# Kernel optimization log

Hardware: AMD Instinct MI355X
Metric: run time of the kernel (lower is better)

## Reference

```python
import jax, jax.numpy as jnp
import numpy as np

B, SQ, SKV, D = 16, 4096, 4096, 64

def setup_inputs() -> dict:
    key = jax.random.key(0)
    kq, kk, kv, ks = jax.random.split(key, 4)
    return {
        "q": jax.random.normal(kq, (B, SQ, D), dtype=jnp.float32),
        "k": jax.random.normal(kk, (B, SKV, D), dtype=jnp.float32),
        "v": jax.random.normal(kv, (B, SKV, D), dtype=jnp.float32),
        "scale_factor": jax.random.uniform(ks, (1,), dtype=jnp.float32, minval=0.05, maxval=0.2),
    }

def reference(q, k, v, scale_factor):
    # qk = q @ k^T, then divide by inv_scale = 1/scale  ==  multiply by scale
    scores = jnp.einsum("bqd,bkd->bqk", q, k) * scale_factor[0]  # [B, SQ, SKV]
    probs = jax.nn.softmax(scores, axis=-1)
    # dropout p=0.0 -> identity (source's p=1 would zero the output; see notes)
    out = jnp.einsum("bqk,bkd->bqd", probs, v)  # [B, SQ, D]
    return out
```

## Files before the change

### kernel.cpp

```cpp
#include <hip/hip_runtime.h>
#include <hip/hip_bf16.h>

#define BATCH 16
#define SEQ   4096
#define DH    64
#define KVB   64
#define NT    (SEQ / KVB)
#define LDK   72

using frag   = __attribute__((ext_vector_type(8))) short;
using f32x16 = __attribute__((ext_vector_type(16))) float;
using u16x8  = __attribute__((ext_vector_type(8))) unsigned short;

__device__ __forceinline__ unsigned short f2bf(float x) {
    union { __hip_bfloat16 h; unsigned short u; } cv;
    cv.h = __float2bfloat16(x);
    return cv.u;
}
__device__ __forceinline__ float bf2f(unsigned short u) {
    union { unsigned int i; float f; } cv;
    cv.i = ((unsigned int)u) << 16;
    return cv.f;
}
__device__ __forceinline__ float fast_exp2(float x) {
#if __has_builtin(__builtin_amdgcn_exp2f)
    return __builtin_amdgcn_exp2f(x);
#else
    float r; asm("v_exp_f32 %0, %1" : "=v"(r) : "v"(x)); return r;
#endif
}
__device__ __forceinline__ unsigned int cvtpk_bf16(float lo, float hi) {
    unsigned int r;
    asm("v_cvt_pk_bf16_f32 %0, %1, %2" : "=v"(r) : "v"(lo), "v"(hi));
    return r;
}
__device__ __forceinline__ void glds16(const unsigned short* g, unsigned short* l) {
    __builtin_amdgcn_global_load_lds(
        (const __attribute__((address_space(1))) void*)g,
        (__attribute__((address_space(3))) void*)l, 16, 0, 0);
}
__device__ __forceinline__ f32x16 mfma32(frag a, frag b, f32x16 c) {
    return __builtin_amdgcn_mfma_f32_32x32x16_bf16(a, b, c, 0, 0, 0);
}

__global__ __launch_bounds__(256) void cvt_k_frag(const float* __restrict__ K,
                                                  unsigned short* __restrict__ Kws) {
    __shared__ unsigned short Ls[64 * LDK];
    const int b = blockIdx.x >> 6;
    const int t = blockIdx.x & 63;
    const int i = threadIdx.x;
    {
        const int kv = i >> 2, db = (i & 3) * 16;
        const float* src = K + ((size_t)b * SEQ + (size_t)t * 64 + kv) * DH + db;
        float4 a = *(const float4*)(src);
        float4 c = *(const float4*)(src + 4);
        float4 d = *(const float4*)(src + 8);
        float4 e = *(const float4*)(src + 12);
        u16x8 w0, w1;
        w0[0]=f2bf(a.x); w0[1]=f2bf(a.y); w0[2]=f2bf(a.z); w0[3]=f2bf(a.w);
        w0[4]=f2bf(c.x); w0[5]=f2bf(c.y); w0[6]=f2bf(c.z); w0[7]=f2bf(c.w);
        w1[0]=f2bf(d.x); w1[1]=f2bf(d.y); w1[2]=f2bf(d.z); w1[3]=f2bf(d.w);
        w1[4]=f2bf(e.x); w1[5]=f2bf(e.y); w1[6]=f2bf(e.z); w1[7]=f2bf(e.w);
        *(u16x8*)&Ls[kv * LDK + db]     = w0;
        *(u16x8*)&Ls[kv * LDK + db + 8] = w1;
    }
    __syncthreads();
    {
        const int flat0 = i * 2;
        const int f     = flat0 >> 6;
        const int kb    = f & 1, kstep = f >> 1;
        const int l0    = flat0 & 63, l1 = l0 + 1;
        u16x8 o0 = *(const u16x8*)&Ls[(kb*32 + (l0&31)) * LDK + kstep*16 + (l0>>5)*8];
        u16x8 o1 = *(const u16x8*)&Ls[(kb*32 + (l1&31)) * LDK + kstep*16 + (l1>>5)*8];
        unsigned short* dst = Kws + ((((size_t)b*64 + t)*8 + f)*64 + l0)*8;
        *(u16x8*)dst       = o0;
        *(u16x8*)(dst + 8) = o1;
    }
}

__global__ __launch_bounds__(256) void tr_v_frag(const float* __restrict__ V,
                                                 unsigned short* __restrict__ Vws) {
    __shared__ unsigned short Ls[64 * LDK];
    const int b = blockIdx.x >> 6;
    const int t = blockIdx.x & 63;
    const int i = threadIdx.x;
    {
        const int kv = i >> 2, db = (i & 3) * 16;
        const float* src = V + ((size_t)b * SEQ + (size_t)t * 64 + kv) * DH + db;
        float4 a = *(const float4*)(src);
        float4 c = *(const float4*)(src + 4);
        float4 d = *(const float4*)(src + 8);
        float4 e = *(const float4*)(src + 12);
        u16x8 w0, w1;
        w0[0]=f2bf(a.x); w0[1]=f2bf(a.y); w0[2]=f2bf(a.z); w0[3]=f2bf(a.w);
        w0[4]=f2bf(c.x); w0[5]=f2bf(c.y); w0[6]=f2bf(c.z); w0[7]=f2bf(c.w);
        w1[0]=f2bf(d.x); w1[1]=f2bf(d.y); w1[2]=f2bf(d.z); w1[3]=f2bf(d.w);
        w1[4]=f2bf(e.x); w1[5]=f2bf(e.y); w1[6]=f2bf(e.z); w1[7]=f2bf(e.w);
        *(u16x8*)&Ls[kv * LDK + db]     = w0;
        *(u16x8*)&Ls[kv * LDK + db + 8] = w1;
    }
    __syncthreads();
    {
        const int flat0 = i * 2;
        const int fv    = flat0 >> 6;
        const int kb    = fv >> 2, ks = (fv >> 1) & 1, dblk = fv & 1;
        u16x8 o0, o1;
        const int l0 = flat0 & 63, l1 = l0 + 1;
#pragma unroll
        for (int j = 0; j < 8; ++j)
            o0[j] = Ls[(kb*32 + ks*16 + (l0>>5)*8 + j) * LDK + dblk*32 + (l0&31)];
#pragma unroll
        for (int j = 0; j < 8; ++j)
            o1[j] = Ls[(kb*32 + ks*16 + (l1>>5)*8 + j) * LDK + dblk*32 + (l1&31)];
        unsigned short* dst = Vws + ((((size_t)b*64 + t)*8 + fv)*64 + l0)*8;
        *(u16x8*)dst       = o0;
        *(u16x8*)(dst + 8) = o1;
    }
}

__global__ __launch_bounds__(256, 4) void attn_fwd(
    const float* __restrict__ Q, const unsigned short* __restrict__ Kws,
    const unsigned short* __restrict__ Vws, const float* __restrict__ S,
    float* __restrict__ O0, unsigned short* __restrict__ O0b,
    unsigned short* __restrict__ O1b,
    float* __restrict__ l0p, float* __restrict__ l1p, int nsplit)
{
    __shared__ unsigned short Kbuf[2][8 * 64 * 8];
    __shared__ unsigned short Vbuf[2][8 * 64 * 8];

    const int bid = blockIdx.x;
    const int xcd = bid & 7;
    int sub = bid >> 3;
    int half = 0;
    if (nsplit == 2) { half = sub & 1; sub >>= 1; }
    const int batch = xcd | ((sub & 1) << 3);
    const int qt    = sub >> 1;

    const int tid  = threadIdx.x;
    const int w    = tid >> 6;
    const int lane = tid & 63;
    const int c32  = lane & 31;
    const int hi   = lane >> 5;

    const int t0   = half * (NT / 2);
    const int ntil = NT / nsplit;

    const float sc = S[0] * 1.44269504088896340736f;

    const float*          Qb = Q   + ((size_t)batch * SEQ + (size_t)qt * 128 + w * 32) * DH;
    const unsigned short* Kg = Kws + (size_t)batch * 64 * 8 * 512;
    const unsigned short* Vg = Vws + (size_t)batch * 64 * 8 * 512;

    frag qF[4];
#pragma unroll
    for (int kstep = 0; kstep < 4; ++kstep) {
        const float* p = Qb + c32 * DH + kstep * 16 + hi * 8;
        float4 a = *(const float4*)p;
        float4 b = *(const float4*)(p + 4);
        frag f;
        f[0] = (short)f2bf(a.x * sc); f[1] = (short)f2bf(a.y * sc);
        f[2] = (short)f2bf(a.z * sc); f[3] = (short)f2bf(a.w * sc);
        f[4] = (short)f2bf(b.x * sc); f[5] = (short)f2bf(b.y * sc);
        f[6] = (short)f2bf(b.z * sc); f[7] = (short)f2bf(b.w * sc);
        qF[kstep] = f;
    }

    frag ones;
#pragma unroll
    for (int j = 0; j < 8; ++j) ones[j] = (short)0x3F80;

    f32x16 o32[2];
    f32x16 l32;
    o32[0] = (f32x16)0.0f; o32[1] = (f32x16)0.0f; l32 = (f32x16)0.0f;

    const int fbase = w * 2;
#pragma unroll
    for (int f = 0; f < 2; ++f) {
        glds16(Kg + (size_t)t0 * 4096 + (fbase + f) * 512 + lane * 8, &Kbuf[0][(fbase + f) * 512]);
        glds16(Vg + (size_t)t0 * 4096 + (fbase + f) * 512 + lane * 8, &Vbuf[0][(fbase + f) * 512]);
    }
    asm volatile("s_waitcnt vmcnt(0)" ::: "memory");
    __builtin_amdgcn_s_barrier();
    __builtin_amdgcn_sched_barrier(0);

    for (int tt = 0; tt < ntil; ++tt) {
        const int t   = t0 + tt;
        const int cur = tt & 1;
        if (tt + 1 < ntil) {
#pragma unroll
            for (int f = 0; f < 2; ++f) {
                glds16(Kg + (size_t)(t + 1) * 4096 + (fbase + f) * 512 + lane * 8,
                       &Kbuf[cur ^ 1][(fbase + f) * 512]);
                glds16(Vg + (size_t)(t + 1) * 4096 + (fbase + f) * 512 + lane * 8,
                       &Vbuf[cur ^ 1][(fbase + f) * 512]);
            }
        }

        f32x16 st[2];
        st[0] = (f32x16)0.0f; st[1] = (f32x16)0.0f;
#pragma unroll
        for (int kstep = 0; kstep < 4; ++kstep)
#pragma unroll
          for (int kb = 0; kb < 2; ++kb) {
            frag kf = *(const frag*)&Kbuf[cur][(kstep * 2 + kb) * 512 + lane * 8];
            st[kb] = mfma32(kf, qF[kstep], st[kb]);
          }

        frag pa[2][2];
#pragma unroll
        for (int kb = 0; kb < 2; ++kb) {
            float p[16];
#pragma unroll
            for (int r = 0; r < 16; ++r) p[r] = fast_exp2(st[kb][r]);
            unsigned a0 = cvtpk_bf16(p[0],  p[1]),  a1 = cvtpk_bf16(p[2],  p[3]);
            unsigned b0 = cvtpk_bf16(p[4],  p[5]),  b1 = cvtpk_bf16(p[6],  p[7]);
            unsigned c0 = cvtpk_bf16(p[8],  p[9]),  c1 = cvtpk_bf16(p[10], p[11]);
            unsigned d0 = cvtpk_bf16(p[12], p[13]), d1 = cvtpk_bf16(p[14], p[15]);
            asm("v_permlane32_swap_b32 %0, %1" : "+v"(a0), "+v"(b0));
            asm("v_permlane32_swap_b32 %0, %1" : "+v"(a1), "+v"(b1));
            asm("v_permlane32_swap_b32 %0, %1" : "+v"(c0), "+v"(d0));
            asm("v_permlane32_swap_b32 %0, %1" : "+v"(c1), "+v"(d1));
            union { unsigned u[4]; frag f; } f0, f1;
            f0.u[0] = a0; f0.u[1] = a1; f0.u[2] = b0; f0.u[3] = b1;
            f1.u[0] = c0; f1.u[1] = c1; f1.u[2] = d0; f1.u[3] = d1;
            pa[kb][0] = f0.f;
            pa[kb][1] = f1.f;
        }

#pragma unroll
        for (int kb = 0; kb < 2; ++kb)
#pragma unroll
          for (int ks = 0; ks < 2; ++ks) {
            l32 = mfma32(pa[kb][ks], ones, l32);
#pragma unroll
            for (int dblk = 0; dblk < 2; ++dblk) {
                frag vf = *(const frag*)&Vbuf[cur][((kb * 2 + ks) * 2 + dblk) * 512 + lane * 8];
                o32[dblk] = mfma32(pa[kb][ks], vf, o32[dblk]);
            }
          }

        asm volatile("s_waitcnt vmcnt(0)" ::: "memory");
        __builtin_amdgcn_s_barrier();
        __builtin_amdgcn_sched_barrier(0);
    }

    const size_t qrow0 = (size_t)batch * SEQ + (size_t)qt * 128 + w * 32;
    if (nsplit == 1) {
        float* Ob = O0 + qrow0 * DH;
        float inv[16];
#pragma unroll
        for (int r = 0; r < 16; ++r) inv[r] = 1.0f / l32[r];
#pragma unroll
        for (int dblk = 0; dblk < 2; ++dblk)
#pragma unroll
          for (int r = 0; r < 16; ++r) {
            const int qrow = (r & 3) + 8 * (r >> 2) + 4 * hi;
            Ob[qrow * DH + dblk * 32 + c32] = o32[dblk][r] * inv[r];
          }
    } else {
        unsigned short* Ob = (half ? O1b : O0b) + qrow0 * DH;
        float* lb = (half ? l1p : l0p) + qrow0;
#pragma unroll
        for (int dblk = 0; dblk < 2; ++dblk)
#pragma unroll
          for (int r = 0; r < 16; ++r) {
            const int qrow = (r & 3) + 8 * (r >> 2) + 4 * hi;
            Ob[qrow * DH + dblk * 32 + c32] = f2bf(o32[dblk][r]);
          }
        if (c32 == 0) {
#pragma unroll
            for (int r = 0; r < 16; ++r) {
                const int qrow = (r & 3) + 8 * (r >> 2) + 4 * hi;
                lb[qrow] = l32[r];
            }
        }
    }
}

__global__ __launch_bounds__(256) void merge_halves(
    float* __restrict__ O, const unsigned short* __restrict__ O0b,
    const unsigned short* __restrict__ O1b,
    const float* __restrict__ l0, const float* __restrict__ l1)
{
    const size_t i0  = ((size_t)blockIdx.x * 256 + threadIdx.x) * 8;
    const size_t row = i0 >> 6;
    const float inv  = 1.0f / (l0[row] + l1[row]);
    u16x8 a = *(const u16x8*)(O0b + i0);
    u16x8 b = *(const u16x8*)(O1b + i0);
    float4 r0, r1;
    r0.x = (bf2f(a[0]) + bf2f(b[0])) * inv;
    r0.y = (bf2f(a[1]) + bf2f(b[1])) * inv;
    r0.z = (bf2f(a[2]) + bf2f(b[2])) * inv;
    r0.w = (bf2f(a[3]) + bf2f(b[3])) * inv;
    r1.x = (bf2f(a[4]) + bf2f(b[4])) * inv;
    r1.y = (bf2f(a[5]) + bf2f(b[5])) * inv;
    r1.z = (bf2f(a[6]) + bf2f(b[6])) * inv;
    r1.w = (bf2f(a[7]) + bf2f(b[7])) * inv;
    *(float4*)(O + i0)     = r0;
    *(float4*)(O + i0 + 4) = r1;
}

extern "C" void kernel_launch(void* const* d_in, const int* in_sizes, int n_in,
                              void* d_out, int out_size, void* d_ws, size_t ws_size,
                              hipStream_t stream) {
    const float* q = (const float*)d_in[0];
    const float* k = (const float*)d_in[1];
    const float* v = (const float*)d_in[2];
    const float* s = (const float*)d_in[3];
    float* o = (float*)d_out;

    const size_t kv_elems = (size_t)BATCH * SEQ * DH;
    unsigned short* kws = (unsigned short*)d_ws;
    unsigned short* vws = kws + kv_elems;
    unsigned short* o0b = vws + kv_elems;
    unsigned short* o1b = o0b + kv_elems;
    float* l0 = (float*)(o1b + kv_elems);
    float* l1 = l0 + (size_t)BATCH * SEQ;
    const size_t need = kv_elems * 2 * 4 + (size_t)BATCH * SEQ * 8;

    cvt_k_frag<<<dim3(BATCH * 64), dim3(256), 0, stream>>>(k, kws);
    tr_v_frag <<<dim3(BATCH * 64), dim3(256), 0, stream>>>(v, vws);

    if (ws_size >= need) {
        attn_fwd<<<dim3(1024), dim3(256), 0, stream>>>(q, kws, vws, s, o, o0b, o1b, l0, l1, 2);
        merge_halves<<<dim3((BATCH * SEQ * DH) / (256 * 8)), dim3(256), 0, stream>>>(o, o0b, o1b, l0, l1);
    } else {
        attn_fwd<<<dim3(512), dim3(256), 0, stream>>>(q, kws, vws, s, o, nullptr, nullptr, nullptr, nullptr, 1);
    }
}
```

Measured before the change: 100.3 us.

## Merge K/V prep kernels and load V fragments directly into registers

```diff
diff --git a/kernel.cpp b/kernel.cpp
--- a/kernel.cpp
+++ b/kernel.cpp
@@ -43,15 +43,19 @@
     return __builtin_amdgcn_mfma_f32_32x32x16_bf16(a, b, c, 0, 0, 0);
 }
 
-__global__ __launch_bounds__(256) void cvt_k_frag(const float* __restrict__ K,
-                                                  unsigned short* __restrict__ Kws) {
+__global__ __launch_bounds__(256) void prep_kv(const float* __restrict__ K,
+                                               const float* __restrict__ V,
+                                               unsigned short* __restrict__ Kws,
+                                               unsigned short* __restrict__ Vws) {
     __shared__ unsigned short Ls[64 * LDK];
-    const int b = blockIdx.x >> 6;
-    const int t = blockIdx.x & 63;
+    const bool isV = blockIdx.x >= (BATCH * 64);
+    const int  bt  = isV ? (blockIdx.x - BATCH * 64) : blockIdx.x;
+    const int b = bt >> 6;
+    const int t = bt & 63;
     const int i = threadIdx.x;
     {
         const int kv = i >> 2, db = (i & 3) * 16;
-        const float* src = K + ((size_t)b * SEQ + (size_t)t * 64 + kv) * DH + db;
+        const float* src = (isV ? V : K) + ((size_t)b * SEQ + (size_t)t * 64 + kv) * DH + db;
         float4 a = *(const float4*)(src);
         float4 c = *(const float4*)(src + 4);
         float4 d = *(const float4*)(src + 8);
@@ -65,7 +69,7 @@
         *(u16x8*)&Ls[kv * LDK + db + 8] = w1;
     }
     __syncthreads();
-    {
+    if (!isV) {
         const int flat0 = i * 2;
         const int f     = flat0 >> 6;
         const int kb    = f & 1, kstep = f >> 1;
@@ -75,32 +79,7 @@
         unsigned short* dst = Kws + ((((size_t)b*64 + t)*8 + f)*64 + l0)*8;
         *(u16x8*)dst       = o0;
         *(u16x8*)(dst + 8) = o1;
-    }
-}
-
-__global__ __launch_bounds__(256) void tr_v_frag(const float* __restrict__ V,
-                                                 unsigned short* __restrict__ Vws) {
-    __shared__ unsigned short Ls[64 * LDK];
-    const int b = blockIdx.x >> 6;
-    const int t = blockIdx.x & 63;
-    const int i = threadIdx.x;
-    {
-        const int kv = i >> 2, db = (i & 3) * 16;
-        const float* src = V + ((size_t)b * SEQ + (size_t)t * 64 + kv) * DH + db;
-        float4 a = *(const float4*)(src);
-        float4 c = *(const float4*)(src + 4);
-        float4 d = *(const float4*)(src + 8);
-        float4 e = *(const float4*)(src + 12);
-        u16x8 w0, w1;
-        w0[0]=f2bf(a.x); w0[1]=f2bf(a.y); w0[2]=f2bf(a.z); w0[3]=f2bf(a.w);
-        w0[4]=f2bf(c.x); w0[5]=f2bf(c.y); w0[6]=f2bf(c.z); w0[7]=f2bf(c.w);
-        w1[0]=f2bf(d.x); w1[1]=f2bf(d.y); w1[2]=f2bf(d.z); w1[3]=f2bf(d.w);
-        w1[4]=f2bf(e.x); w1[5]=f2bf(e.y); w1[6]=f2bf(e.z); w1[7]=f2bf(e.w);
-        *(u16x8*)&Ls[kv * LDK + db]     = w0;
-        *(u16x8*)&Ls[kv * LDK + db + 8] = w1;
-    }
-    __syncthreads();
-    {
+    } else {
         const int flat0 = i * 2;
         const int fv    = flat0 >> 6;
         const int kb    = fv >> 2, ks = (fv >> 1) & 1, dblk = fv & 1;
@@ -126,7 +105,6 @@
     float* __restrict__ l0p, float* __restrict__ l1p, int nsplit)
 {
     __shared__ unsigned short Kbuf[2][8 * 64 * 8];
-    __shared__ unsigned short Vbuf[2][8 * 64 * 8];
 
     const int bid = blockIdx.x;
     const int xcd = bid & 7;
@@ -175,10 +153,8 @@
 
     const int fbase = w * 2;
 #pragma unroll
-    for (int f = 0; f < 2; ++f) {
+    for (int f = 0; f < 2; ++f)
         glds16(Kg + (size_t)t0 * 4096 + (fbase + f) * 512 + lane * 8, &Kbuf[0][(fbase + f) * 512]);
-        glds16(Vg + (size_t)t0 * 4096 + (fbase + f) * 512 + lane * 8, &Vbuf[0][(fbase + f) * 512]);
-    }
     asm volatile("s_waitcnt vmcnt(0)" ::: "memory");
     __builtin_amdgcn_s_barrier();
     __builtin_amdgcn_sched_barrier(0);
@@ -186,14 +162,18 @@
     for (int tt = 0; tt < ntil; ++tt) {
         const int t   = t0 + tt;
         const int cur = tt & 1;
+
+        const unsigned short* Vt = Vg + (size_t)t * 4096;
+        frag vf[8];
+#pragma unroll
+        for (int f = 0; f < 8; ++f)
+            vf[f] = *(const frag*)(Vt + f * 512 + lane * 8);
+
         if (tt + 1 < ntil) {
 #pragma unroll
-            for (int f = 0; f < 2; ++f) {
+            for (int f = 0; f < 2; ++f)
                 glds16(Kg + (size_t)(t + 1) * 4096 + (fbase + f) * 512 + lane * 8,
                        &Kbuf[cur ^ 1][(fbase + f) * 512]);
-                glds16(Vg + (size_t)(t + 1) * 4096 + (fbase + f) * 512 + lane * 8,
-                       &Vbuf[cur ^ 1][(fbase + f) * 512]);
-            }
         }
 
         f32x16 st[2];
@@ -233,10 +213,8 @@
           for (int ks = 0; ks < 2; ++ks) {
             l32 = mfma32(pa[kb][ks], ones, l32);
 #pragma unroll
-            for (int dblk = 0; dblk < 2; ++dblk) {
-                frag vf = *(const frag*)&Vbuf[cur][((kb * 2 + ks) * 2 + dblk) * 512 + lane * 8];
-                o32[dblk] = mfma32(pa[kb][ks], vf, o32[dblk]);
-            }
+            for (int dblk = 0; dblk < 2; ++dblk)
+                o32[dblk] = mfma32(pa[kb][ks], vf[(kb * 2 + ks) * 2 + dblk], o32[dblk]);
           }
 
         asm volatile("s_waitcnt vmcnt(0)" ::: "memory");
@@ -318,8 +296,7 @@
     float* l1 = l0 + (size_t)BATCH * SEQ;
     const size_t need = kv_elems * 2 * 4 + (size_t)BATCH * SEQ * 8;
 
-    cvt_k_frag<<<dim3(BATCH * 64), dim3(256), 0, stream>>>(k, kws);
-    tr_v_frag <<<dim3(BATCH * 64), dim3(256), 0, stream>>>(v, vws);
+    prep_kv<<<dim3(2 * BATCH * 64), dim3(256), 0, stream>>>(k, v, kws, vws);
 
     if (ws_size >= need) {
         attn_fwd<<<dim3(1024), dim3(256), 0, stream>>>(q, kws, vws, s, o, o0b, o1b, l0, l1, 2);
```

Result: slower. 137.2 us (+36.7%).
